# Kernel tuning notes

Measured on AMD Instinct MI355X. Metric: run time of the kernel, lower is better.

The kernel has to match this reference:

```python
import jax, jax.numpy as jnp
import numpy as np

GROUP_SIZE = 128  # vLLM machete default group size
ZERO_POINT = 8.0  # uint4b8: stored unsigned 4-bit, logical value = q - 8


def setup_inputs() -> dict:
    key = jax.random.key(0)
    k_a, k_b, k_s = jax.random.split(key, 3)
    M, K, N = 4096, 4096, 12288
    a = jax.random.normal(k_a, (M, K), dtype=jnp.float32)
    # int4 quantized weights stored as small ints in [0, 16)
    b_q = jax.random.randint(k_b, (K, N), 0, 16, dtype=jnp.int32)
    # per-group scales: one scale per (group of 128 rows of K) per output column
    scales = jax.random.uniform(k_s, (K // GROUP_SIZE, N), dtype=jnp.float32) * 0.02 + 0.001
    return {"a": a, "b_q": b_q, "scales": scales}


def reference(a, b_q, scales):
    K, N = b_q.shape
    G = K // GROUP_SIZE
    # dequantize: (q - 8) * group_scale, scale broadcast over each K-group
    b = (b_q.astype(jnp.float32) - ZERO_POINT).reshape(G, GROUP_SIZE, N)
    b = (b * scales[:, None, :]).reshape(K, N)  # [K, N] dequantized weights
    return a @ b  # [M, N]
```

## Files before the change

### kernel.cpp

```cpp
#include <hip/hip_runtime.h>
#include <hip/hip_bf16.h>
#include <stdint.h>

constexpr int Mdim = 4096;
constexpr int Kdim = 4096;
constexpr int Ndim = 12288;

constexpr int NKT = Kdim / 64;
constexpr int GM256 = Mdim / 256;
constexpr int GN256 = Ndim / 256;
constexpr int NWG256 = GM256 * GN256;
constexpr int GRID_M = Mdim / 128;
constexpr int GRID_N = Ndim / 128;
constexpr int NWG = GRID_M * GRID_N;

typedef float  f32x4   __attribute__((ext_vector_type(4)));
typedef __bf16 bf16x4v __attribute__((ext_vector_type(4)));
typedef __bf16 bf16x8v __attribute__((ext_vector_type(8)));
typedef int    i32x4   __attribute__((ext_vector_type(4)));
typedef unsigned short ushort8 __attribute__((ext_vector_type(8)));

typedef __attribute__((address_space(3))) uint32_t       lds_u32;
typedef __attribute__((address_space(1))) const uint32_t glb_u32;

__device__ __forceinline__ void gload16(const void* g, void* l) {
    __builtin_amdgcn_global_load_lds((glb_u32*)(uintptr_t)g,
                                     (lds_u32*)(uint32_t)(uintptr_t)l, 16, 0, 0);
}


__launch_bounds__(256)
__global__ void cvtA(const float* __restrict__ A, unsigned short* __restrict__ Aw) {
    int t = blockIdx.x * 256 + threadIdx.x;
    int r = t >> 9;
    int c = t & 511;
    const float* src = A + ((long)r << 12) + (c << 3);
    f32x4 v0 = *(const f32x4*)src;
    f32x4 v1 = *(const f32x4*)(src + 4);
    bf16x8v o;
#pragma unroll
    for (int j = 0; j < 4; ++j) { o[j] = (__bf16)v0[j]; o[4 + j] = (__bf16)v1[j]; }
    int ks = c & 3;
    int cp = (c & ~3) | (ks ^ ((r >> 1) & 3));
    *(bf16x8v*)(Aw + ((long)r << 12) + (cp << 3)) = o;
}

__launch_bounds__(256)
__global__ void deqB(const int* __restrict__ Bq, const float* __restrict__ S,
                     unsigned short* __restrict__ Bw) {
    __shared__ unsigned short lt[64][72];
    int kb = blockIdx.x & 63;
    int nb = blockIdx.x >> 6;
    int k0 = kb << 6, n0 = nb << 6;
    int tid = threadIdx.x;
    int g = k0 >> 7;
    int nq = (tid & 15) << 2;
    f32x4 sc = *(const f32x4*)(S + (long)g * Ndim + n0 + nq);
#pragma unroll
    for (int p = 0; p < 4; ++p) {
        int kk = (p << 4) + (tid >> 4);
        i32x4 q = *(const i32x4*)(Bq + (long)(k0 + kk) * Ndim + n0 + nq);
#pragma unroll
        for (int j = 0; j < 4; ++j) {
            float v = ((float)q[j] - 8.f) * sc[j];
            lt[nq + j][kk] = __builtin_bit_cast(unsigned short, (__bf16)v);
        }
    }
    __syncthreads();
#pragma unroll
    for (int h = 0; h < 2; ++h) {
        int cidx = tid + (h << 8);
        int n = cidx >> 3, sidx = cidx & 7;
        int kh = sidx >> 2, ks = sidx & 3;
        int ksp = ks ^ ((n >> 1) & 3);
        ushort8 v = *(const ushort8*)&lt[n][sidx << 3];
        *(ushort8*)(Bw + (long)(n0 + n) * Kdim + k0 + kh * 32 + ksp * 8) = v;
    }
}

__device__ __forceinline__ void mfma16(const bf16x8v* a4, const bf16x8v* b4,
                                       f32x4 (*acc)[4]) {
#pragma unroll
    for (int m = 0; m < 4; ++m)
#pragma unroll
        for (int n = 0; n < 4; ++n)
            acc[m][n] = __builtin_amdgcn_mfma_f32_16x16x32_bf16(a4[m], b4[n], acc[m][n], 0, 0, 0);
}

__launch_bounds__(512, 2)
__global__ void gemm256(const unsigned short* __restrict__ Aw,
                        const unsigned short* __restrict__ Bw,
                        float* __restrict__ C) {
    extern __shared__ unsigned char ldsbuf[];

    const int tid  = threadIdx.x;
    const int lane = tid & 63;
    const int w    = tid >> 6;
    const int wr   = w >> 2, wc = w & 3;
    const int fr   = lane & 15;
    const int ks   = lane >> 4;

    const int bid = blockIdx.x;
    const int xcd = bid & 7;
    const int loc = bid >> 3;
    const int pn  = loc >> 4;
    const int tm  = loc & 15;
    const int tn  = xcd * 6 + pn;
    const int brow = tm << 8, bcol = tn << 8;

    const unsigned char* baseA = (const unsigned char*)Aw
        + (size_t)(brow + (tid >> 2)) * 8192 + (size_t)(tid & 3) * 16;
    const unsigned char* baseB = (const unsigned char*)Bw
        + (size_t)(bcol + (tid >> 2)) * 8192 + (size_t)(tid & 3) * 16;

    int offA[8][2], offB[4][2];
#pragma unroll
    for (int am = 0; am < 8; ++am)
#pragma unroll
        for (int kh = 0; kh < 2; ++kh) {
            int rowL = wr * 128 + am * 16 + fr;
            offA[am][kh] = (kh << 14) + rowL * 64 + ((ks ^ ((rowL >> 1) & 3)) << 4);
        }
#pragma unroll
    for (int n = 0; n < 4; ++n)
#pragma unroll
        for (int kh = 0; kh < 2; ++kh) {
            int colL = wc * 64 + n * 16 + fr;
            offB[n][kh] = (kh << 14) + colL * 64 + ((ks ^ ((colL >> 1) & 3)) << 4);
        }

    auto stageA = [&](int tile, int kh) {
        if (tile < NKT) {
            const unsigned char* s = baseA + (size_t)tile * 128 + (kh << 6);
            unsigned char* d = ldsbuf + ((tile & 1) << 16) + (kh << 14) + (w << 10);
            gload16(s, d);
            gload16(s + 1048576, d + 8192);
        }
    };
    auto stageB = [&](int tile, int kh) {
        if (tile < NKT) {
            const unsigned char* s = baseB + (size_t)tile * 128 + (kh << 6);
            unsigned char* d = ldsbuf + ((tile & 1) << 16) + 32768 + (kh << 14) + (w << 10);
            gload16(s, d);
            gload16(s + 1048576, d + 8192);
        }
    };

    f32x4 accT[4][4], accB[4][4];
#pragma unroll
    for (int m = 0; m < 4; ++m)
#pragma unroll
        for (int n = 0; n < 4; ++n) {
            accT[m][n] = (f32x4){0.f, 0.f, 0.f, 0.f};
            accB[m][n] = (f32x4){0.f, 0.f, 0.f, 0.f};
        }

    stageA(0, 0); stageB(0, 0); stageA(0, 1); stageB(0, 1);
    stageA(1, 0); stageB(1, 0);
    asm volatile("s_waitcnt vmcnt(4)" ::: "memory");
    __builtin_amdgcn_s_barrier();

    bf16x8v A0[4], A1[4], A2[4], B0[4], B1[4];

    for (int T = 0; T < NKT; ++T) {
        unsigned char* sAc = ldsbuf + ((T & 1) << 16);
        unsigned char* sBc = sAc + 32768;

#pragma unroll
        for (int m = 0; m < 4; ++m) A0[m] = *(const bf16x8v*)(sAc + offA[m][0]);
#pragma unroll
        for (int n = 0; n < 4; ++n) B0[n] = *(const bf16x8v*)(sBc + offB[n][0]);
#pragma unroll
        for (int m = 0; m < 4; ++m) A1[m] = *(const bf16x8v*)(sAc + offA[4 + m][0]);
        stageA(T + 1, 1);
        __builtin_amdgcn_s_barrier();
        __builtin_amdgcn_s_setprio(1);
        mfma16(A0, B0, accT);
        __builtin_amdgcn_s_setprio(0);
        __builtin_amdgcn_s_barrier();

#pragma unroll
        for (int n = 0; n < 4; ++n) B1[n] = *(const bf16x8v*)(sBc + offB[n][1]);
#pragma unroll
        for (int m = 0; m < 4; ++m) A2[m] = *(const bf16x8v*)(sAc + offA[m][1]);
        stageB(T + 1, 1);
        __builtin_amdgcn_s_barrier();
        __builtin_amdgcn_s_setprio(1);
        mfma16(A1, B0, accB);
        __builtin_amdgcn_s_setprio(0);
        __builtin_amdgcn_s_barrier();

#pragma unroll
        for (int m = 0; m < 4; ++m) A0[m] = *(const bf16x8v*)(sAc + offA[4 + m][1]);
        stageA(T + 2, 0);
        __builtin_amdgcn_s_barrier();
        __builtin_amdgcn_s_setprio(1);
        mfma16(A2, B1, accT);
        __builtin_amdgcn_s_setprio(0);
        __builtin_amdgcn_s_barrier();

        stageB(T + 2, 0);
        __builtin_amdgcn_s_barrier();
        __builtin_amdgcn_s_setprio(1);
        mfma16(A0, B1, accB);
        __builtin_amdgcn_s_setprio(0);
        if (T < NKT - 2) asm volatile("s_waitcnt vmcnt(4)" ::: "memory");
        else             asm volatile("s_waitcnt vmcnt(0)" ::: "memory");
        __builtin_amdgcn_s_barrier();
    }

#pragma unroll
    for (int am = 0; am < 8; ++am) {
        int row = brow + wr * 128 + am * 16 + ks * 4;
#pragma unroll
        for (int n = 0; n < 4; ++n) {
            int col = bcol + wc * 64 + n * 16 + fr;
            f32x4 v = (am < 4) ? accT[am & 3][n] : accB[am & 3][n];
            float* cp = C + (long)row * Ndim + col;
#pragma unroll
            for (int r = 0; r < 4; ++r) cp[(long)r * Ndim] = v[r];
        }
    }
}

__launch_bounds__(256, 3)
__global__ void gemm_bf16(const unsigned short* __restrict__ Aw,
                          const unsigned short* __restrict__ Bw,
                          float* __restrict__ C) {
    __shared__ unsigned char sA[128 * 64 * 2];
    __shared__ unsigned char sB[128 * 64 * 2];

    const int tid  = threadIdx.x;
    const int lane = tid & 63;
    const int w    = tid >> 6;

    const int bid   = blockIdx.x;
    const int x     = bid & 7;
    const int local = bid >> 3;
    const int pn    = local >> 5;
    const int tm    = local & 31;
    const int tn    = x * 12 + pn;
    const int brow  = tm << 7;
    const int bcol  = tn << 7;

    const unsigned char* ga[4];
    const unsigned char* gb[4];
#pragma unroll
    for (int i = 0; i < 4; ++i) {
        int c = (w << 8) + (i << 6) + lane;
        int r = c >> 3, s = c & 7;
        ga[i] = (const unsigned char*)Aw + (long)(brow + r) * 8192 + (s << 4);
        gb[i] = (const unsigned char*)Bw + (long)(bcol + r) * 8192 + (s << 4);
    }

    const int fr = lane & 15;
    const int ks = lane >> 4;
    const int wr = w >> 1, wc = w & 1;
    int ra[4][2], rb[4][2];
#pragma unroll
    for (int m = 0; m < 4; ++m)
#pragma unroll
        for (int kk = 0; kk < 2; ++kk) {
            int r_a = wr * 64 + m * 16 + fr;
            int r_b = wc * 64 + m * 16 + fr;
            ra[m][kk] = (r_a << 7) + (kk << 6) + ((ks ^ ((r_a >> 1) & 3)) << 4);
            rb[m][kk] = (r_b << 7) + (kk << 6) + ((ks ^ ((r_b >> 1) & 3)) << 4);
        }

    f32x4 acc[4][4];
#pragma unroll
    for (int m = 0; m < 4; ++m)
#pragma unroll
        for (int n = 0; n < 4; ++n) acc[m][n] = (f32x4){0.f, 0.f, 0.f, 0.f};

    for (int kt = 0; kt < NKT; ++kt) {
#pragma unroll
        for (int i = 0; i < 4; ++i) {
            gload16(ga[i], sA + (((w << 2) + i) << 10));
            gload16(gb[i], sB + (((w << 2) + i) << 10));
            ga[i] += 128;
            gb[i] += 128;
        }
        __syncthreads();

#pragma unroll
        for (int kk = 0; kk < 2; ++kk) {
            bf16x8v af[4], bf[4];
#pragma unroll
            for (int m = 0; m < 4; ++m) af[m] = *(const bf16x8v*)(sA + ra[m][kk]);
#pragma unroll
            for (int n = 0; n < 4; ++n) bf[n] = *(const bf16x8v*)(sB + rb[n][kk]);
#pragma unroll
            for (int m = 0; m < 4; ++m)
#pragma unroll
                for (int n = 0; n < 4; ++n)
                    acc[m][n] = __builtin_amdgcn_mfma_f32_16x16x32_bf16(af[m], bf[n], acc[m][n], 0, 0, 0);
        }
        __syncthreads();
    }

#pragma unroll
    for (int m = 0; m < 4; ++m) {
        int row = brow + wr * 64 + m * 16 + ks * 4;
#pragma unroll
        for (int n = 0; n < 4; ++n) {
            int col = bcol + wc * 64 + n * 16 + fr;
            f32x4 v = acc[m][n];
            float* cp = C + (long)row * Ndim + col;
#pragma unroll
            for (int r = 0; r < 4; ++r) cp[(long)r * Ndim] = v[r];
        }
    }
}

__device__ __forceinline__ int swz_f(int row, int kbyte) {
    int s = kbyte >> 4;
    int f = s ^ ((row ^ (row >> 2)) & 7);
    return (row << 7) + (f << 4) + (kbyte & 15);
}

__launch_bounds__(256, 2)
__global__ void machete_fused(const float* __restrict__ A,
                              const int* __restrict__ Bq,
                              const float* __restrict__ S,
                              float* __restrict__ C) {
    __shared__ unsigned char sA[128 * 64 * 2];
    __shared__ unsigned char sB[128 * 64 * 2];

    const int tid = threadIdx.x;
    const int bid = blockIdx.x;
    const int sid = (bid & 7) * (NWG / 8) + (bid >> 3);
    const int tm = sid / GRID_N;
    const int tn = sid % GRID_N;
    const int brow = tm * 128;
    const int bcol = tn * 128;

    const int a_row0 = tid >> 4;
    const int a_kb   = tid & 15;
    const int b_kb = tid >> 4;
    const int b_nb = tid & 15;

    int aw[8];
#pragma unroll
    for (int i = 0; i < 8; ++i) aw[i] = swz_f(a_row0 + 16 * i, a_kb * 8);
    int bw[2][4];
#pragma unroll
    for (int i = 0; i < 2; ++i)
#pragma unroll
        for (int j = 0; j < 4; ++j) bw[i][j] = swz_f(4 * b_nb + 64 * i + j, b_kb * 8);

    const int lane = tid & 63;
    const int w  = tid >> 6;
    const int wr = w >> 1, wc = w & 1;
    const int fr = lane & 15;
    const int ks = lane >> 4;
    int ar[4][2], br[4][2];
#pragma unroll
    for (int m = 0; m < 4; ++m)
#pragma unroll
        for (int kk = 0; kk < 2; ++kk) {
            ar[m][kk] = swz_f(wr * 64 + m * 16 + fr, kk * 64 + ks * 16);
            br[m][kk] = swz_f(wc * 64 + m * 16 + fr, kk * 64 + ks * 16);
        }

    const float* Ap = A + (long)brow * Kdim;
    const int*   Bp = Bq + bcol;

    f32x4 aregs[8];
    i32x4 bregs[2][4];
    f32x4 sregs[2];

#pragma unroll
    for (int i = 0; i < 8; ++i)
        aregs[i] = *(const f32x4*)(Ap + (long)(a_row0 + 16 * i) * Kdim + a_kb * 4);
#pragma unroll
    for (int i = 0; i < 2; ++i) {
#pragma unroll
        for (int r = 0; r < 4; ++r)
            bregs[i][r] = *(const i32x4*)(Bp + (long)(b_kb * 4 + r) * Ndim + 4 * b_nb + 64 * i);
        sregs[i] = *(const f32x4*)(S + bcol + 4 * b_nb + 64 * i);
    }

    f32x4 acc[4][4];
#pragma unroll
    for (int m = 0; m < 4; ++m)
#pragma unroll
        for (int n = 0; n < 4; ++n) acc[m][n] = (f32x4){0.f, 0.f, 0.f, 0.f};

    for (int kt = 0; kt < NKT; ++kt) {
#pragma unroll
        for (int i = 0; i < 8; ++i) {
            f32x4 v = aregs[i];
            bf16x4v p;
            p[0] = (__bf16)v[0]; p[1] = (__bf16)v[1];
            p[2] = (__bf16)v[2]; p[3] = (__bf16)v[3];
            *(bf16x4v*)(sA + aw[i]) = p;
        }
#pragma unroll
        for (int i = 0; i < 2; ++i) {
            f32x4 sc = sregs[i];
#pragma unroll
            for (int j = 0; j < 4; ++j) {
                float scj = sc[j];
                float nm8 = -8.f * scj;
                bf16x4v p;
#pragma unroll
                for (int r = 0; r < 4; ++r) {
                    float v = (float)bregs[i][r][j] * scj + nm8;
                    p[r] = (__bf16)v;
                }
                *(bf16x4v*)(sB + bw[i][j]) = p;
            }
        }
        __syncthreads();

        if (kt + 1 < NKT) {
            const float* Ap2 = Ap + (kt + 1) * 64;
            const int*   Bp2 = Bq + bcol + (long)((kt + 1) * 64) * Ndim;
            const float* Sp2 = S + (long)((kt + 1) >> 1) * Ndim + bcol;
#pragma unroll
            for (int i = 0; i < 8; ++i)
                aregs[i] = *(const f32x4*)(Ap2 + (long)(a_row0 + 16 * i) * Kdim + a_kb * 4);
#pragma unroll
            for (int i = 0; i < 2; ++i) {
#pragma unroll
                for (int r = 0; r < 4; ++r)
                    bregs[i][r] = *(const i32x4*)(Bp2 + (long)(b_kb * 4 + r) * Ndim + 4 * b_nb + 64 * i);
                sregs[i] = *(const f32x4*)(Sp2 + 4 * b_nb + 64 * i);
            }
        }

#pragma unroll
        for (int kk = 0; kk < 2; ++kk) {
            bf16x8v af[4], bfv[4];
#pragma unroll
            for (int m = 0; m < 4; ++m) af[m] = *(const bf16x8v*)(sA + ar[m][kk]);
#pragma unroll
            for (int n = 0; n < 4; ++n) bfv[n] = *(const bf16x8v*)(sB + br[n][kk]);
#pragma unroll
            for (int m = 0; m < 4; ++m)
#pragma unroll
                for (int n = 0; n < 4; ++n)
                    acc[m][n] = __builtin_amdgcn_mfma_f32_16x16x32_bf16(af[m], bfv[n], acc[m][n], 0, 0, 0);
        }
        __syncthreads();
    }

#pragma unroll
    for (int m = 0; m < 4; ++m) {
        int row = brow + wr * 64 + m * 16 + ks * 4;
#pragma unroll
        for (int n = 0; n < 4; ++n) {
            int col = bcol + wc * 64 + n * 16 + fr;
            f32x4 v = acc[m][n];
            float* cp = C + (long)row * Ndim + col;
#pragma unroll
            for (int r = 0; r < 4; ++r) cp[(long)r * Ndim] = v[r];
        }
    }
}

extern "C" void kernel_launch(void* const* d_in, const int* in_sizes, int n_in,
                              void* d_out, int out_size, void* d_ws, size_t ws_size,
                              hipStream_t stream) {
    const float* A  = (const float*)d_in[0];
    const int*   Bq = (const int*)d_in[1];
    const float* S  = (const float*)d_in[2];
    float* C = (float*)d_out;

    const size_t a_elems = (size_t)Mdim * Kdim;
    const size_t b_elems = (size_t)Ndim * Kdim;
    const size_t need = (a_elems + b_elems) * sizeof(unsigned short);

    if (ws_size >= need) {
        unsigned short* Aw = (unsigned short*)d_ws;
        unsigned short* Bw = Aw + a_elems;
        hipLaunchKernelGGL(cvtA, dim3((Mdim * Kdim / 8) / 256), dim3(256), 0, stream, A, Aw);
        hipLaunchKernelGGL(deqB, dim3((Kdim / 64) * (Ndim / 64)), dim3(256), 0, stream, Bq, S, Bw);
        hipError_t e = hipFuncSetAttribute(
            reinterpret_cast<const void*>(gemm256),
            hipFuncAttributeMaxDynamicSharedMemorySize, 131072);
        if (e == hipSuccess) {
            hipLaunchKernelGGL(gemm256, dim3(NWG256), dim3(512), 131072, stream, Aw, Bw, C);
        } else {
            hipLaunchKernelGGL(gemm_bf16, dim3(NWG), dim3(256), 0, stream, Aw, Bw, C);
        }
    } else {
        hipLaunchKernelGGL(machete_fused, dim3(NWG), dim3(256), 0, stream, A, Bq, S, C);
    }
}
```

Measured before the change: 463.4 us.

## Switch gemm256 to 32x32x16 MFMA with restructured two-phase pipelined K loop

Replaces the 16x16x32 bf16 MFMA tiling in the 256x256 GEMM kernel with 32x32x16 MFMA fragments (4x2 per wave, f32x16 accumulators). The K loop is unrolled by two tiles, halving barriers per tile and issuing all four A/B staging loads together with a single waitcnt. The aim is fewer LDS reads per FLOP and less sync overhead, but correctness depends on the new swizzled offsets and output index mapping, and register pressure shifts.

Result: slower. 495.3 us (+6.9%).

```diff
diff --git a/kernel.cpp b/kernel.cpp
--- a/kernel.cpp
+++ b/kernel.cpp
@@ -15,6 +15,7 @@
 constexpr int NWG = GRID_M * GRID_N;
 
 typedef float  f32x4   __attribute__((ext_vector_type(4)));
+typedef float  f32x16  __attribute__((ext_vector_type(16)));
 typedef __bf16 bf16x4v __attribute__((ext_vector_type(4)));
 typedef __bf16 bf16x8v __attribute__((ext_vector_type(8)));
 typedef int    i32x4   __attribute__((ext_vector_type(4)));
@@ -78,15 +79,6 @@
     }
 }
 
-__device__ __forceinline__ void mfma16(const bf16x8v* a4, const bf16x8v* b4,
-                                       f32x4 (*acc)[4]) {
-#pragma unroll
-    for (int m = 0; m < 4; ++m)
-#pragma unroll
-        for (int n = 0; n < 4; ++n)
-            acc[m][n] = __builtin_amdgcn_mfma_f32_16x16x32_bf16(a4[m], b4[n], acc[m][n], 0, 0, 0);
-}
-
 __launch_bounds__(512, 2)
 __global__ void gemm256(const unsigned short* __restrict__ Aw,
                         const unsigned short* __restrict__ Bw,
@@ -97,8 +89,8 @@
     const int lane = tid & 63;
     const int w    = tid >> 6;
     const int wr   = w >> 2, wc = w & 3;
-    const int fr   = lane & 15;
-    const int ks   = lane >> 4;
+    const int l31  = lane & 31;
+    const int l5   = lane >> 5;
 
     const int bid = blockIdx.x;
     const int xcd = bid & 7;
@@ -108,119 +100,136 @@
     const int tn  = xcd * 6 + pn;
     const int brow = tm << 8, bcol = tn << 8;
 
-    const unsigned char* baseA = (const unsigned char*)Aw
+    const unsigned char* pA  = (const unsigned char*)Aw
         + (size_t)(brow + (tid >> 2)) * 8192 + (size_t)(tid & 3) * 16;
-    const unsigned char* baseB = (const unsigned char*)Bw
+    const unsigned char* pA2 = pA + (size_t)128 * 8192;
+    const unsigned char* pB  = (const unsigned char*)Bw
         + (size_t)(bcol + (tid >> 2)) * 8192 + (size_t)(tid & 3) * 16;
-
-    int offA[8][2], offB[4][2];
-#pragma unroll
-    for (int am = 0; am < 8; ++am)
-#pragma unroll
-        for (int kh = 0; kh < 2; ++kh) {
-            int rowL = wr * 128 + am * 16 + fr;
-            offA[am][kh] = (kh << 14) + rowL * 64 + ((ks ^ ((rowL >> 1) & 3)) << 4);
-        }
-#pragma unroll
-    for (int n = 0; n < 4; ++n)
-#pragma unroll
-        for (int kh = 0; kh < 2; ++kh) {
-            int colL = wc * 64 + n * 16 + fr;
-            offB[n][kh] = (kh << 14) + colL * 64 + ((ks ^ ((colL >> 1) & 3)) << 4);
-        }
-
-    auto stageA = [&](int tile, int kh) {
-        if (tile < NKT) {
-            const unsigned char* s = baseA + (size_t)tile * 128 + (kh << 6);
-            unsigned char* d = ldsbuf + ((tile & 1) << 16) + (kh << 14) + (w << 10);
-            gload16(s, d);
-            gload16(s + 1048576, d + 8192);
-        }
-    };
-    auto stageB = [&](int tile, int kh) {
-        if (tile < NKT) {
-            const unsigned char* s = baseB + (size_t)tile * 128 + (kh << 6);
-            unsigned char* d = ldsbuf + ((tile & 1) << 16) + 32768 + (kh << 14) + (w << 10);
-            gload16(s, d);
-            gload16(s + 1048576, d + 8192);
-        }
-    };
-
-    f32x4 accT[4][4], accB[4][4];
-#pragma unroll
-    for (int m = 0; m < 4; ++m)
-#pragma unroll
-        for (int n = 0; n < 4; ++n) {
-            accT[m][n] = (f32x4){0.f, 0.f, 0.f, 0.f};
-            accB[m][n] = (f32x4){0.f, 0.f, 0.f, 0.f};
-        }
-
-    stageA(0, 0); stageB(0, 0); stageA(0, 1); stageB(0, 1);
-    stageA(1, 0); stageB(1, 0);
+    const unsigned char* pB2 = pB + (size_t)128 * 8192;
+
+    const int ldw = w << 10;
+
+    int offA[4][4], offB[2][4];
+#pragma unroll
+    for (int mf = 0; mf < 4; ++mf)
+#pragma unroll
+        for (int q = 0; q < 4; ++q) {
+            int rowL = wr * 128 + mf * 32 + l31;
+            int s = ((q & 1) << 1) + l5;
+            offA[mf][q] = ((q >> 1) << 14) + rowL * 64 + ((s ^ ((rowL >> 1) & 3)) << 4);
+        }
+#pragma unroll
+    for (int nf = 0; nf < 2; ++nf)
+#pragma unroll
+        for (int q = 0; q < 4; ++q) {
+            int colL = wc * 64 + nf * 32 + l31;
+            int s = ((q & 1) << 1) + l5;
+            offB[nf][q] = ((q >> 1) << 14) + colL * 64 + ((s ^ ((colL >> 1) & 3)) << 4);
+        }
+
+    f32x16 acc[4][2];
+#pragma unroll
+    for (int mf = 0; mf < 4; ++mf)
+#pragma unroll
+        for (int nf = 0; nf < 2; ++nf)
+#pragma unroll
+            for (int e = 0; e < 16; ++e) acc[mf][nf][e] = 0.f;
+
+#define STAGE4(dstb, soff)                                                    \
+    gload16(pA  + (soff), ldsbuf + (dstb) + ldw);                             \
+    gload16(pA2 + (soff), ldsbuf + (dstb) + ldw + 8192);                      \
+    gload16(pB  + (soff), ldsbuf + (dstb) + 32768 + ldw);                     \
+    gload16(pB2 + (soff), ldsbuf + (dstb) + 32768 + ldw + 8192);
+
+#define RD(base, off) (*(const bf16x8v*)((base) + (off)))
+
+#define MFMA8(Aset, Bset)                                                     \
+    _Pragma("unroll")                                                         \
+    for (int mf = 0; mf < 4; ++mf)                                            \
+        _Pragma("unroll")                                                     \
+        for (int nf = 0; nf < 2; ++nf)                                        \
+            acc[mf][nf] = __builtin_amdgcn_mfma_f32_32x32x16_bf16(            \
+                (Aset)[mf], (Bset)[nf], acc[mf][nf], 0, 0, 0);
+
+#define TILE_BODY(BUF, SO, DO_STAGE1, DO_STAGE2, VM)                          \
+    {                                                                         \
+        unsigned char* sAc = ldsbuf + ((BUF) << 16);                          \
+        unsigned char* sBc = sAc + 32768;                                     \
+        bf16x8v a0[4], a1[4], b0[2], b1[2];                                   \
+        _Pragma("unroll") for (int nf = 0; nf < 2; ++nf) {                    \
+            b0[nf] = RD(sBc, offB[nf][0]); b1[nf] = RD(sBc, offB[nf][1]); }   \
+        _Pragma("unroll") for (int mf = 0; mf < 4; ++mf) {                    \
+            a0[mf] = RD(sAc, offA[mf][0]); a1[mf] = RD(sAc, offA[mf][1]); }   \
+        if (DO_STAGE1) { STAGE4(((1 - (BUF)) << 16) + (1 << 14), (SO) + 192) }\
+        __builtin_amdgcn_s_setprio(1);                                        \
+        MFMA8(a0, b0)                                                         \
+        MFMA8(a1, b1)                                                         \
+        __builtin_amdgcn_s_setprio(0);                                        \
+        __builtin_amdgcn_s_barrier();                                         \
+        _Pragma("unroll") for (int nf = 0; nf < 2; ++nf) {                    \
+            b0[nf] = RD(sBc, offB[nf][2]); b1[nf] = RD(sBc, offB[nf][3]); }   \
+        _Pragma("unroll") for (int mf = 0; mf < 4; ++mf) {                    \
+            a0[mf] = RD(sAc, offA[mf][2]); a1[mf] = RD(sAc, offA[mf][3]); }   \
+        if (DO_STAGE2) { STAGE4(((BUF) << 16), (SO) + 256) }                  \
+        __builtin_amdgcn_s_setprio(1);                                        \
+        MFMA8(a0, b0)                                                         \
+        MFMA8(a1, b1)                                                         \
+        __builtin_amdgcn_s_setprio(0);                                        \
+        asm volatile("s_waitcnt vmcnt(" #VM ")" ::: "memory");                \
+        __builtin_amdgcn_s_barrier();                                         \
+    }
+
+    STAGE4(0, 0)
+    STAGE4((1 << 14), 64)
+    STAGE4((1 << 16), 128)
     asm volatile("s_waitcnt vmcnt(4)" ::: "memory");
     __builtin_amdgcn_s_barrier();
 
-    bf16x8v A0[4], A1[4], A2[4], B0[4], B1[4];
-
-    for (int T = 0; T < NKT; ++T) {
-        unsigned char* sAc = ldsbuf + ((T & 1) << 16);
+    for (int T = 0; T < NKT - 2; T += 2) {
+        TILE_BODY(0, 0, 1, 1, 4)
+        TILE_BODY(1, 128, 1, 1, 4)
+        pA += 256; pA2 += 256; pB += 256; pB2 += 256;
+    }
+    TILE_BODY(0, 0, 1, 0, 0)
+    {
+        unsigned char* sAc = ldsbuf + (1 << 16);
         unsigned char* sBc = sAc + 32768;
-
-#pragma unroll
-        for (int m = 0; m < 4; ++m) A0[m] = *(const bf16x8v*)(sAc + offA[m][0]);
-#pragma unroll
-        for (int n = 0; n < 4; ++n) B0[n] = *(const bf16x8v*)(sBc + offB[n][0]);
-#pragma unroll
-        for (int m = 0; m < 4; ++m) A1[m] = *(const bf16x8v*)(sAc + offA[4 + m][0]);
-        stageA(T + 1, 1);
-        __builtin_amdgcn_s_barrier();
-        __builtin_amdgcn_s_setprio(1);
-        mfma16(A0, B0, accT);
-        __builtin_amdgcn_s_setprio(0);
-        __builtin_amdgcn_s_barrier();
-
-#pragma unroll
-        for (int n = 0; n < 4; ++n) B1[n] = *(const bf16x8v*)(sBc + offB[n][1]);
-#pragma unroll
-        for (int m = 0; m < 4; ++m) A2[m] = *(const bf16x8v*)(sAc + offA[m][1]);
-        stageB(T + 1, 1);
-        __builtin_amdgcn_s_barrier();
-        __builtin_amdgcn_s_setprio(1);
-        mfma16(A1, B0, accB);
-        __builtin_amdgcn_s_setprio(0);
-        __builtin_amdgcn_s_barrier();
-
-#pragma unroll
-        for (int m = 0; m < 4; ++m) A0[m] = *(const bf16x8v*)(sAc + offA[4 + m][1]);
-        stageA(T + 2, 0);
-        __builtin_amdgcn_s_barrier();
-        __builtin_amdgcn_s_setprio(1);
-        mfma16(A2, B1, accT);
-        __builtin_amdgcn_s_setprio(0);
-        __builtin_amdgcn_s_barrier();
-
-        stageB(T + 2, 0);
-        __builtin_amdgcn_s_barrier();
-        __builtin_amdgcn_s_setprio(1);
-        mfma16(A0, B1, accB);
-        __builtin_amdgcn_s_setprio(0);
-        if (T < NKT - 2) asm volatile("s_waitcnt vmcnt(4)" ::: "memory");
-        else             asm volatile("s_waitcnt vmcnt(0)" ::: "memory");
-        __builtin_amdgcn_s_barrier();
-    }
-
-#pragma unroll
-    for (int am = 0; am < 8; ++am) {
-        int row = brow + wr * 128 + am * 16 + ks * 4;
-#pragma unroll
-        for (int n = 0; n < 4; ++n) {
-            int col = bcol + wc * 64 + n * 16 + fr;
-            f32x4 v = (am < 4) ? accT[am & 3][n] : accB[am & 3][n];
-            float* cp = C + (long)row * Ndim + col;
-#pragma unroll
-            for (int r = 0; r < 4; ++r) cp[(long)r * Ndim] = v[r];
-        }
-    }
+        bf16x8v a0[4], a1[4], b0[2], b1[2];
+#pragma unroll
+        for (int q2 = 0; q2 < 4; q2 += 2) {
+#pragma unroll
+            for (int nf = 0; nf < 2; ++nf) {
+                b0[nf] = RD(sBc, offB[nf][q2]); b1[nf] = RD(sBc, offB[nf][q2 + 1]);
+            }
+#pragma unroll
+            for (int mf = 0; mf < 4; ++mf) {
+                a0[mf] = RD(sAc, offA[mf][q2]); a1[mf] = RD(sAc, offA[mf][q2 + 1]);
+            }
+            MFMA8(a0, b0)
+            MFMA8(a1, b1)
+        }
+    }
+
+#pragma unroll
+    for (int mf = 0; mf < 4; ++mf)
+#pragma unroll
+        for (int nf = 0; nf < 2; ++nf) {
+            f32x16 v = acc[mf][nf];
+            int col = bcol + wc * 64 + nf * 32 + l31;
+#pragma unroll
+            for (int g = 0; g < 4; ++g) {
+                int row = brow + wr * 128 + mf * 32 + 8 * g + 4 * l5;
+                float* cp = C + (size_t)row * Ndim + col;
+                cp[0] = v[4 * g + 0];
+                cp[(size_t)Ndim] = v[4 * g + 1];
+                cp[(size_t)2 * Ndim] = v[4 * g + 2];
+                cp[(size_t)3 * Ndim] = v[4 * g + 3];
+            }
+        }
+#undef TILE_BODY
+#undef MFMA8
+#undef RD
+#undef STAGE4
 }
 
 __launch_bounds__(256, 3)
```
